# Optimization experiments

Hardware: AMD Instinct MI355X
Metric: run time of the kernel (lower is better)

Reference implementation:

```python
import jax, jax.numpy as jnp
import numpy as np

N_NODES = 20000
N_ANCHORS = 64
D_IN = 128
D_OUT = 128
N_EDGES = N_NODES * N_ANCHORS  # 1,280,000


def setup_inputs() -> dict:
    key = jax.random.key(0)
    ks = jax.random.split(key, 8)
    feature = jax.random.normal(ks[0], (N_NODES, D_IN), dtype=jnp.float32)
    sp_dist = jax.random.uniform(ks[1], (N_EDGES,), dtype=jnp.float32)
    # xavier_uniform with relu gain ~ sqrt(2)*sqrt(6/(fan_in+fan_out))
    def xavier(k, fan_in, fan_out):
        bound = jnp.sqrt(2.0) * jnp.sqrt(6.0 / (fan_in + fan_out))
        return jax.random.uniform(k, (fan_in, fan_out), dtype=jnp.float32,
                                  minval=-bound, maxval=bound)
    Wu = xavier(ks[2], D_IN, D_OUT)
    Wv = xavier(ks[3], D_IN, D_OUT)
    Wpos = xavier(ks[4], D_OUT, 1)
    bu = jnp.zeros((D_OUT,), jnp.float32)
    bv = jnp.zeros((D_OUT,), jnp.float32)
    bpos = jnp.zeros((1,), jnp.float32)
    src = jax.random.randint(ks[5], (N_EDGES,), 0, N_NODES, dtype=jnp.int32)
    dst = jax.random.randint(ks[6], (N_EDGES,), 0, N_NODES, dtype=jnp.int32)
    anchor_eid = jax.random.randint(ks[7], (N_EDGES,), 0, N_EDGES, dtype=jnp.int32)
    return {"feature": feature, "sp_dist": sp_dist, "Wu": Wu, "bu": bu,
            "Wv": Wv, "bv": bv, "Wpos": Wpos, "bpos": bpos,
            "src": src, "dst": dst, "anchor_eid": anchor_eid}


def reference(feature, sp_dist, Wu, bu, Wv, bv, Wpos, bpos, src, dst, anchor_eid):
    # Dense projections of node features (linear_hidden_u / linear_hidden_v)
    u_feat = feature @ Wu + bu  # [N, D_OUT]
    v_feat = feature @ Wv + bv  # [N, D_OUT]
    # apply_edges u_mul_e + v_add_e, then index_select on anchor edges.
    # Gathering at anchor edges directly computes the same values as
    # computing all edge messages and then selecting the anchor subset.
    s = src[anchor_eid]            # [E]
    d = dst[anchor_eid]            # [E]
    sp = sp_dist[anchor_eid]       # [E]
    messages = u_feat[s] * sp[:, None] + v_feat[d]       # [E, D_OUT]
    messages = jax.nn.relu(messages).reshape(N_NODES, N_ANCHORS, D_OUT)
    out_position = (messages @ Wpos + bpos)[..., 0]      # [N, K]
    out_structure = messages.mean(axis=1)                # [N, D_OUT]
    return out_position, out_structure
```

## Files before the change

kernel.cpp:

```cpp
#include <hip/hip_runtime.h>

#define N_NODES   20000
#define N_ANCHORS 64
#define D         128
#define N_EDGES   (N_NODES * N_ANCHORS)
#define NCHUNK    4
#define CDIM      32

typedef float f32x2  __attribute__((ext_vector_type(2)));
typedef float f32x4  __attribute__((ext_vector_type(4)));
typedef short bf16x8 __attribute__((ext_vector_type(8)));

static __device__ __forceinline__ unsigned short f32_to_bf16(float x) {
    unsigned int u = __float_as_uint(x);
    u += 0x7FFFu + ((u >> 16) & 1u);
    return (unsigned short)(u >> 16);
}
static __device__ __forceinline__ f32x2 bf2(unsigned int w) {
    f32x2 r;
    r.x = __uint_as_float(w << 16);
    r.y = __uint_as_float(w & 0xFFFF0000u);
    return r;
}

#define NB_PACK    (N_EDGES / 256)
#define NB_WCVT    ((D * D) / 256)
#define NB_PREFILL (N_EDGES / 1024)
__global__ __launch_bounds__(256) void prep_kernel(
    const int* __restrict__ src, const int* __restrict__ dst,
    const float* __restrict__ sp_dist,
    const float* __restrict__ Wu, const float* __restrict__ Wv,
    const float* __restrict__ bpos,
    unsigned long long* __restrict__ epack,
    unsigned short* __restrict__ Wt_u, unsigned short* __restrict__ Wt_v,
    float* __restrict__ out_pos)
{
    const int bid = blockIdx.x;
    if (bid < NB_PACK) {
        const int e = bid * 256 + threadIdx.x;
        const unsigned int s = (unsigned int)__builtin_nontemporal_load(&src[e]);
        const unsigned int d = (unsigned int)__builtin_nontemporal_load(&dst[e]);
        const float       sp = __builtin_nontemporal_load(&sp_dist[e]);
        epack[e] = (unsigned long long)(s | (d << 15)) |
                   ((unsigned long long)__float_as_uint(sp) << 32);
    } else if (bid < NB_PACK + NB_WCVT) {
        const int t = (bid - NB_PACK) * 256 + threadIdx.x;
        const int k = t >> 7, j = t & 127;
        Wt_u[j * D + k] = f32_to_bf16(Wu[t]);
        Wt_v[j * D + k] = f32_to_bf16(Wv[t]);
    } else {
        const int i = (bid - NB_PACK - NB_WCVT) * 256 + threadIdx.x;
        const float bp = bpos[0];
        f32x4 v = {bp, bp, bp, bp};
        __builtin_nontemporal_store(v, (f32x4*)out_pos + i);
    }
}

__global__ __launch_bounds__(256) void meta_kernel(
    const unsigned long long* __restrict__ epack,
    const int* __restrict__ anchor_eid,
    unsigned long long* __restrict__ meta)
{
    const int e = blockIdx.x * 256 + threadIdx.x;
    const int eid = __builtin_nontemporal_load(&anchor_eid[e]);
    const unsigned long long m = epack[eid];
    __builtin_nontemporal_store(m, &meta[e]);
}

__global__ __launch_bounds__(256) void proj_mfma_kernel(
    const float* __restrict__ feature,
    const unsigned short* __restrict__ Wt_u,
    const unsigned short* __restrict__ Wt_v,
    const float* __restrict__ bu, const float* __restrict__ bv,
    unsigned short* __restrict__ u_c, unsigned short* __restrict__ v_c)
{
    const int wave = threadIdx.x >> 6;
    const int lane = threadIdx.x & 63;
    const int n0   = blockIdx.x * 16;
    const int mat    = wave & 1;
    const int ctbase = (wave >> 1) * 4;

    const int row = lane & 15;
    const int kq  = lane >> 4;

    bf16x8 afrag[4];
    #pragma unroll
    for (int kt = 0; kt < 4; ++kt) {
        const float* fp = feature + (size_t)(n0 + row) * D + kt * 32 + kq * 8;
        const f32x4 f0 = *(const f32x4*)fp;
        const f32x4 f1 = *(const f32x4*)(fp + 4);
        bf16x8 a;
        #pragma unroll
        for (int e = 0; e < 4; ++e) a[e]     = (short)f32_to_bf16(f0[e]);
        #pragma unroll
        for (int e = 0; e < 4; ++e) a[4 + e] = (short)f32_to_bf16(f1[e]);
        afrag[kt] = a;
    }

    const unsigned short* Wt   = mat ? Wt_v : Wt_u;
    const float*          bias = mat ? bv   : bu;
    unsigned short*       outp = mat ? v_c  : u_c;

    #pragma unroll
    for (int t = 0; t < 4; ++t) {
        const int ct = ctbase + t;
        const int j  = ct * 16 + row;
        f32x4 acc = {0.f, 0.f, 0.f, 0.f};
        #pragma unroll
        for (int kt = 0; kt < 4; ++kt) {
            const bf16x8 b = *(const bf16x8*)(Wt + (size_t)j * D + kt * 32 + kq * 8);
            acc = __builtin_amdgcn_mfma_f32_16x16x32_bf16(afrag[kt], b, acc, 0, 0, 0);
        }
        const float bj  = bias[j];
        const int  cj   = ct >> 1;
        const int  dimc = (ct & 1) * 16 + row;
        #pragma unroll
        for (int r = 0; r < 4; ++r) {
            const int n = n0 + kq * 4 + r;
            outp[((size_t)cj * N_NODES + n) * CDIM + dimc] = f32_to_bf16(acc[r] + bj);
        }
    }
}

__global__ __launch_bounds__(256) void fused_chunk_kernel(
    const unsigned short* __restrict__ u_c, const unsigned short* __restrict__ v_c,
    const unsigned long long* __restrict__ meta,
    const float* __restrict__ Wpos,
    float* __restrict__ out_pos, float* __restrict__ out_struct)
{
    const int bid   = blockIdx.x;
    const int x     = bid & 7;
    const int chunk = x >> 1;
    const int half  = x & 1;
    const int nb    = bid >> 3;
    const int wave  = threadIdx.x >> 6;
    const int lane  = threadIdx.x & 63;
    const int n     = half * 10000 + nb * 4 + wave;

    const int sub = lane & 3;
    const int grp = lane >> 2;

    const unsigned long long mm =
        __builtin_nontemporal_load(&meta[(size_t)n * N_ANCHORS + lane]);
    const int   s  = (int)(mm & 0x7FFFu);
    const int   d  = (int)((mm >> 15) & 0x7FFFu);
    const float sp = __uint_as_float((unsigned int)(mm >> 32));

    f32x2 wp[4];
    {
        const f32x2* wpp = (const f32x2*)(Wpos + chunk * CDIM + sub * 8);
        #pragma unroll
        for (int q = 0; q < 4; ++q) wp[q] = wpp[q];
    }

    const unsigned short* ub = u_c + (size_t)chunk * N_NODES * CDIM;
    const unsigned short* vb = v_c + (size_t)chunk * N_NODES * CDIM;

    f32x2 acc0 = {0.f, 0.f}, acc1 = {0.f, 0.f}, acc2 = {0.f, 0.f}, acc3 = {0.f, 0.f};
    const f32x2 zero2 = {0.f, 0.f};

    __shared__ float posbuf[4][N_ANCHORS];

    uint4 ubuf[4], vbuf[4];
    {
        const unsigned short* ua[4];
        const unsigned short* va[4];
        #pragma unroll
        for (int it = 0; it < 4; ++it) {
            const int a = it * 16 + grp;
            const int sa = __shfl(s, a);
            const int da = __shfl(d, a);
            ua[it] = ub + (size_t)sa * CDIM + sub * 8;
            va[it] = vb + (size_t)da * CDIM + sub * 8;
        }
        #pragma unroll
        for (int it = 0; it < 4; ++it) {
            asm volatile("global_load_dwordx4 %0, %1, off"
                         : "=v"(ubuf[it]) : "v"(ua[it]));
            asm volatile("global_load_dwordx4 %0, %1, off"
                         : "=v"(vbuf[it]) : "v"(va[it]));
        }
        asm volatile("s_waitcnt vmcnt(0)" ::: "memory");
        __builtin_amdgcn_sched_barrier(0);
    }

    #pragma unroll
    for (int it = 0; it < 4; ++it) {
        const int a = it * 16 + grp;
        const float spa = __shfl(sp, a);
        const uint4 uu = ubuf[it];
        const uint4 vv = vbuf[it];

        f32x2 m0 = bf2(uu.x) * spa + bf2(vv.x);
        f32x2 m1 = bf2(uu.y) * spa + bf2(vv.y);
        f32x2 m2 = bf2(uu.z) * spa + bf2(vv.z);
        f32x2 m3 = bf2(uu.w) * spa + bf2(vv.w);
        m0 = __builtin_elementwise_max(m0, zero2);
        m1 = __builtin_elementwise_max(m1, zero2);
        m2 = __builtin_elementwise_max(m2, zero2);
        m3 = __builtin_elementwise_max(m3, zero2);

        acc0 += m0; acc1 += m1; acc2 += m2; acc3 += m3;

        f32x2 pd = m0 * wp[0] + m1 * wp[1] + m2 * wp[2] + m3 * wp[3];
        float p = pd.x + pd.y;
        p += __shfl_xor(p, 2);
        p += __shfl_xor(p, 1);
        if (sub == 0) posbuf[wave][a] = p;
    }

    float acc[8] = {acc0.x, acc0.y, acc1.x, acc1.y, acc2.x, acc2.y, acc3.x, acc3.y};
    #pragma unroll
    for (int k = 0; k < 8; ++k) {
        acc[k] += __shfl_xor(acc[k], 4);
        acc[k] += __shfl_xor(acc[k], 8);
        acc[k] += __shfl_xor(acc[k], 16);
        acc[k] += __shfl_xor(acc[k], 32);
    }


    atomicAdd(&out_pos[(size_t)n * N_ANCHORS + lane], posbuf[wave][lane]);

    if (grp == 0) {
        const float inv = 1.0f / (float)N_ANCHORS;
        f32x4 o0, o1;
        o0.x = acc[0] * inv; o0.y = acc[1] * inv; o0.z = acc[2] * inv; o0.w = acc[3] * inv;
        o1.x = acc[4] * inv; o1.y = acc[5] * inv; o1.z = acc[6] * inv; o1.w = acc[7] * inv;
        float* os = out_struct + (size_t)n * D + chunk * CDIM + sub * 8;
        __builtin_nontemporal_store(o0, (f32x4*)os);
        __builtin_nontemporal_store(o1, (f32x4*)(os + 4));
    }
}

extern "C" void kernel_launch(void* const* d_in, const int* in_sizes, int n_in,
                              void* d_out, int out_size, void* d_ws, size_t ws_size,
                              hipStream_t stream) {
    const float* feature    = (const float*)d_in[0];
    const float* sp_dist    = (const float*)d_in[1];
    const float* Wu         = (const float*)d_in[2];
    const float* bu         = (const float*)d_in[3];
    const float* Wv         = (const float*)d_in[4];
    const float* bv         = (const float*)d_in[5];
    const float* Wpos       = (const float*)d_in[6];
    const float* bpos       = (const float*)d_in[7];
    const int*   src        = (const int*)d_in[8];
    const int*   dst        = (const int*)d_in[9];
    const int*   anchor_eid = (const int*)d_in[10];

    unsigned short* u_c = (unsigned short*)d_ws;
    unsigned short* v_c = u_c + (size_t)NCHUNK * N_NODES * CDIM;
    unsigned long long* epack = (unsigned long long*)d_ws;
    unsigned long long* meta =
        (unsigned long long*)((char*)d_ws + (size_t)2 * NCHUNK * N_NODES * CDIM * 2);

    float* out_pos    = (float*)d_out;
    float* out_struct = out_pos + (size_t)N_EDGES;

    unsigned short* Wt_u = (unsigned short*)out_struct;
    unsigned short* Wt_v = Wt_u + D * D;

    prep_kernel<<<NB_PACK + NB_WCVT + NB_PREFILL, 256, 0, stream>>>(
        src, dst, sp_dist, Wu, Wv, bpos, epack, Wt_u, Wt_v, out_pos);
    meta_kernel<<<N_EDGES / 256, 256, 0, stream>>>(epack, anchor_eid, meta);
    proj_mfma_kernel<<<N_NODES / 16, 256, 0, stream>>>(feature, Wt_u, Wt_v,
                                                       bu, bv, u_c, v_c);
    fused_chunk_kernel<<<N_NODES * NCHUNK / 4, 256, 0, stream>>>(
        u_c, v_c, meta, Wpos, out_pos, out_struct);
}
```

Measured before the change: 122.0 us.

## Merge meta gather and projection kernels, shrink edge metadata to bf16 distances

The anchor-edge metadata gather and the MFMA projection now run as one launch, with blocks split by index. That removes a kernel launch boundary and lets the two independent stages overlap. Edge metadata is split into a 4-byte src/dst word and a 2-byte bf16 sp_dist, cutting metadata write and read traffic. The epack scratch moves into the out_struct region and the transposed weights move into the workspace, so concurrent writes to u_c no longer clobber data still being read. The bf16 rounding of sp_dist adds numerical error to the messages.

```diff
diff --git a/kernel.cpp b/kernel.cpp
--- a/kernel.cpp
+++ b/kernel.cpp
@@ -56,27 +56,33 @@
     }
 }
 
-__global__ __launch_bounds__(256) void meta_kernel(
-    const unsigned long long* __restrict__ epack,
-    const int* __restrict__ anchor_eid,
-    unsigned long long* __restrict__ meta)
-{
-    const int e = blockIdx.x * 256 + threadIdx.x;
-    const int eid = __builtin_nontemporal_load(&anchor_eid[e]);
-    const unsigned long long m = epack[eid];
-    __builtin_nontemporal_store(m, &meta[e]);
-}
-
-__global__ __launch_bounds__(256) void proj_mfma_kernel(
+#define NB_PROJ (N_NODES / 16)
+#define NB_META (N_EDGES / 256)
+__global__ __launch_bounds__(256) void mega_kernel(
     const float* __restrict__ feature,
     const unsigned short* __restrict__ Wt_u,
     const unsigned short* __restrict__ Wt_v,
     const float* __restrict__ bu, const float* __restrict__ bv,
-    unsigned short* __restrict__ u_c, unsigned short* __restrict__ v_c)
+    unsigned short* __restrict__ u_c, unsigned short* __restrict__ v_c,
+    const unsigned long long* __restrict__ epack,
+    const int* __restrict__ anchor_eid,
+    unsigned int* __restrict__ meta_sd,
+    unsigned short* __restrict__ meta_sp)
 {
+    const int bid = blockIdx.x;
+    if (bid >= NB_PROJ) {
+        const int e = (bid - NB_PROJ) * 256 + threadIdx.x;
+        const int eid = __builtin_nontemporal_load(&anchor_eid[e]);
+        const unsigned long long m = epack[eid];
+        const float sp = __uint_as_float((unsigned int)(m >> 32));
+        __builtin_nontemporal_store((unsigned int)m, &meta_sd[e]);
+        __builtin_nontemporal_store(f32_to_bf16(sp), &meta_sp[e]);
+        return;
+    }
+
     const int wave = threadIdx.x >> 6;
     const int lane = threadIdx.x & 63;
-    const int n0   = blockIdx.x * 16;
+    const int n0   = bid * 16;
     const int mat    = wave & 1;
     const int ctbase = (wave >> 1) * 4;
 
@@ -124,7 +130,8 @@
 
 __global__ __launch_bounds__(256) void fused_chunk_kernel(
     const unsigned short* __restrict__ u_c, const unsigned short* __restrict__ v_c,
-    const unsigned long long* __restrict__ meta,
+    const unsigned int* __restrict__ meta_sd,
+    const unsigned short* __restrict__ meta_sp,
     const float* __restrict__ Wpos,
     float* __restrict__ out_pos, float* __restrict__ out_struct)
 {
@@ -140,11 +147,11 @@
     const int sub = lane & 3;
     const int grp = lane >> 2;
 
-    const unsigned long long mm =
-        __builtin_nontemporal_load(&meta[(size_t)n * N_ANCHORS + lane]);
-    const int   s  = (int)(mm & 0x7FFFu);
-    const int   d  = (int)((mm >> 15) & 0x7FFFu);
-    const float sp = __uint_as_float((unsigned int)(mm >> 32));
+    const unsigned int   sd  = __builtin_nontemporal_load(&meta_sd[(size_t)n * N_ANCHORS + lane]);
+    const unsigned short spw = __builtin_nontemporal_load(&meta_sp[(size_t)n * N_ANCHORS + lane]);
+    const int   s  = (int)(sd & 0x7FFFu);
+    const int   d  = (int)((sd >> 15) & 0x7FFFu);
+    const float sp = __uint_as_float((unsigned int)spw << 16);
 
     f32x2 wp[4];
     {
@@ -249,21 +256,22 @@
 
     unsigned short* u_c = (unsigned short*)d_ws;
     unsigned short* v_c = u_c + (size_t)NCHUNK * N_NODES * CDIM;
-    unsigned long long* epack = (unsigned long long*)d_ws;
-    unsigned long long* meta =
-        (unsigned long long*)((char*)d_ws + (size_t)2 * NCHUNK * N_NODES * CDIM * 2);
+
+    char* regY = (char*)d_ws + (size_t)2 * NCHUNK * N_NODES * CDIM * 2;
+    unsigned int*   meta_sd = (unsigned int*)regY;
+    unsigned short* meta_sp = (unsigned short*)(regY + (size_t)N_EDGES * 4);
+    unsigned short* Wt_u    = (unsigned short*)(regY + (size_t)N_EDGES * 6);
+    unsigned short* Wt_v    = Wt_u + D * D;
 
     float* out_pos    = (float*)d_out;
     float* out_struct = out_pos + (size_t)N_EDGES;
-
-    unsigned short* Wt_u = (unsigned short*)out_struct;
-    unsigned short* Wt_v = Wt_u + D * D;
+    unsigned long long* epack = (unsigned long long*)out_struct;
 
     prep_kernel<<<NB_PACK + NB_WCVT + NB_PREFILL, 256, 0, stream>>>(
         src, dst, sp_dist, Wu, Wv, bpos, epack, Wt_u, Wt_v, out_pos);
-    meta_kernel<<<N_EDGES / 256, 256, 0, stream>>>(epack, anchor_eid, meta);
-    proj_mfma_kernel<<<N_NODES / 16, 256, 0, stream>>>(feature, Wt_u, Wt_v,
-                                                       bu, bv, u_c, v_c);
+    mega_kernel<<<NB_PROJ + NB_META, 256, 0, stream>>>(
+        feature, Wt_u, Wt_v, bu, bv, u_c, v_c, epack, anchor_eid,
+        meta_sd, meta_sp);
     fused_chunk_kernel<<<N_NODES * NCHUNK / 4, 256, 0, stream>>>(
-        u_c, v_c, meta, Wpos, out_pos, out_struct);
-}
+        u_c, v_c, meta_sd, meta_sp, Wpos, out_pos, out_struct);
+}
```

Result: faster. 108.5 us (-11.0%).
